# Optimization experiments

Hardware: AMD Instinct MI355X
Metric: run time of the kernel (lower is better)

## Reference

```python
import jax, jax.numpy as jnp
import numpy as np

N_NODES = 10000
DEG = 16
E = N_NODES * DEG
IN = 256
OUT = 256
B = 2
SLOPE = 0.2


def setup_inputs() -> dict:
    key = jax.random.key(0)
    ks = jax.random.split(key, 8)
    rng = np.random.default_rng(0)
    # edges sorted by source, every node appears as a source exactly DEG times
    src = np.repeat(np.arange(N_NODES, dtype=np.int64), DEG)
    tgt = rng.integers(0, N_NODES, size=E).astype(np.int64)
    # torch.unique(..., return_inverse=True) -> sorted uniques + inverse ids
    usrc, sid = np.unique(src, return_inverse=True)
    utgt, tid = np.unique(tgt, return_inverse=True)
    s = 1.0 / np.sqrt(IN)
    sa = 1.0 / np.sqrt(2 * OUT)
    return {
        "nodes": jax.random.normal(ks[0], (N_NODES, B, IN), jnp.float32),
        "Ws": jax.random.normal(ks[1], (IN, OUT), jnp.float32) * s,
        "bs": jnp.zeros((OUT,), jnp.float32),
        "Wt": jax.random.normal(ks[2], (IN, OUT), jnp.float32) * s,
        "bt": jnp.zeros((OUT,), jnp.float32),
        "Wv": jax.random.normal(ks[3], (IN, OUT), jnp.float32) * s,
        "bv": jnp.zeros((OUT,), jnp.float32),
        "Wa": jax.random.normal(ks[4], (2 * OUT, 1), jnp.float32) * sa,
        "ba": jnp.zeros((1,), jnp.float32),
        "unique_source_node_id": jnp.asarray(usrc),
        "unique_target_node_id": jnp.asarray(utgt),
        "source_id_per_edge": jnp.asarray(sid),
        "target_id_per_edge": jnp.asarray(tid),
    }


def reference(nodes, Ws, bs, Wt, bt, Wv, bv, Wa, ba,
              unique_source_node_id, unique_target_node_id,
              source_id_per_edge, target_id_per_edge):
    Ns = unique_source_node_id.shape[0]
    # project_node_states
    src_proj = nodes[unique_source_node_id] @ Ws + bs          # [Ns, B, O]
    tgt_proj = nodes[unique_target_node_id] @ Wt + bt          # [Nt, B, O]
    # gather_node_pairs + attention + LeakyReLU
    paired = jnp.concatenate(
        [src_proj[source_id_per_edge], tgt_proj[target_id_per_edge]], axis=-1)  # [E, B, 2O]
    scores = jax.nn.leaky_relu(paired @ Wa + ba, SLOPE)        # [E, B, 1]
    # neighbourhood_softmax: exp(clip) then scatter-add over source segments
    ex = jnp.exp(jnp.clip(scores, -2.0, 2.0))
    denom = jax.ops.segment_sum(ex, source_id_per_edge, num_segments=Ns)
    alpha = ex / denom[source_id_per_edge]                     # [E, B, 1]
    # apply_attention (values_type='new')
    vals = nodes[unique_target_node_id] @ Wv + bv              # [Nt, B, O]
    weighted = alpha * vals[target_id_per_edge]                # [E, B, O]
    # aggregate_neighbours: the original indexes the per-edge weighted values
    # by target_id_per_edge along the EDGE axis (faithfully reproduced), then
    # sums contiguous same-source segments.
    gathered = weighted[target_id_per_edge]                    # [E, B, O]
    agg = jax.ops.segment_sum(gathered, source_id_per_edge, num_segments=Ns)
    # update_sources (update_type='sum'), return_only_source_nodes=True
    return src_proj + agg                                      # [Ns, B, O]
```

## Files before the change

### kernel.cpp

```cpp
#include <hip/hip_runtime.h>

#define B2 2
#define DEG 16
#define SLOPE 0.2f

typedef __attribute__((ext_vector_type(8))) short short8;
typedef __attribute__((ext_vector_type(8))) unsigned short ushort8;
typedef __attribute__((ext_vector_type(4))) unsigned short ushort4v;
typedef __attribute__((ext_vector_type(4))) float f32x4;

__device__ inline unsigned short f2bf(float f) {
  union { float f; unsigned u; } v; v.f = f;
  unsigned r = v.u + 0x7fff + ((v.u >> 16) & 1);
  return (unsigned short)(r >> 16);
}
__device__ inline float bf2f(unsigned short u) {
  union { unsigned u; float f; } c; c.u = ((unsigned)u) << 16;
  return c.f;
}

__device__ inline float wave_dot256(const float* __restrict__ a,
                                    const float* __restrict__ b, int lane) {
  float4 x = *(const float4*)(a + lane * 4);
  float4 y = *(const float4*)(b + lane * 4);
  float v = x.x * y.x + x.y * y.y + x.z * y.z + x.w * y.w;
  #pragma unroll
  for (int off = 32; off; off >>= 1) v += __shfl_down(v, off);
  return v;
}

__global__ __launch_bounds__(256) void prep_w_k(
    const float* __restrict__ Ws, const float* __restrict__ Wt,
    const float* __restrict__ Wv, const float* __restrict__ Wa,
    const float* __restrict__ bs, const float* __restrict__ bt,
    unsigned short* __restrict__ WsT, unsigned short* __restrict__ WvT,
    float* __restrict__ ws_comb, float* __restrict__ wt_comb,
    float* __restrict__ consts) {
  int bx = blockIdx.x;
  if (bx < 32) {
    const float* src = (bx & 16) ? Wv : Ws;
    unsigned short* dst = (bx & 16) ? WvT : WsT;
    int rc = bx & 15;
    int r0 = (rc >> 2) * 64, c0 = (rc & 3) * 64;
    __shared__ float tile[64][65];
    int tr = threadIdx.x >> 6, tc = threadIdx.x & 63;
    #pragma unroll
    for (int i = 0; i < 16; ++i) {
      int r = tr * 16 + i;
      tile[r][tc] = src[(long)(r0 + r) * 256 + c0 + tc];
    }
    __syncthreads();
    #pragma unroll
    for (int i = 0; i < 16; ++i) {
      int r = tr * 16 + i;
      dst[(long)(c0 + r) * 256 + r0 + tc] = f2bf(tile[tc][r]);
    }
  } else {
    int wave = (bx - 32) * 4 + (threadIdx.x >> 6);
    int lane = threadIdx.x & 63;
    if (wave >= 514) return;
    const float *vec, *wa;
    float* dst;
    if (wave < 256)       { vec = Ws + (long)wave * 256;         wa = Wa;       dst = ws_comb + wave; }
    else if (wave < 512)  { vec = Wt + (long)(wave - 256) * 256; wa = Wa + 256; dst = wt_comb + (wave - 256); }
    else if (wave == 512) { vec = bs; wa = Wa;       dst = consts; }
    else                  { vec = bt; wa = Wa + 256; dst = consts + 1; }
    float v = wave_dot256(vec, wa, lane);
    if (lane == 0) *dst = v;
  }
}

__global__ __launch_bounds__(256) void prep_nodes_k(
    const float* __restrict__ nodes, const float* __restrict__ ws_comb,
    const float* __restrict__ wt_comb, unsigned short* __restrict__ nodes_bf,
    float* __restrict__ an_s, float* __restrict__ an_t, int nrows) {
  int wave = blockIdx.x * 4 + (threadIdx.x >> 6);
  int lane = threadIdx.x & 63;
  if (wave >= nrows) return;
  const float4 a = *(const float4*)(nodes + (long)wave * 256 + lane * 4);
  ushort4v p;
  p[0] = f2bf(a.x); p[1] = f2bf(a.y); p[2] = f2bf(a.z); p[3] = f2bf(a.w);
  *(ushort4v*)(nodes_bf + (long)wave * 256 + lane * 4) = p;
  const float4 w1 = *(const float4*)(ws_comb + lane * 4);
  const float4 w2 = *(const float4*)(wt_comb + lane * 4);
  float vs = a.x * w1.x + a.y * w1.y + a.z * w1.z + a.w * w1.w;
  float vt = a.x * w2.x + a.y * w2.y + a.z * w2.z + a.w * w2.w;
  #pragma unroll
  for (int off = 32; off; off >>= 1) {
    vs += __shfl_down(vs, off);
    vt += __shfl_down(vt, off);
  }
  if (lane == 0) { an_s[wave] = vs; an_t[wave] = vt; }
}

__global__ __launch_bounds__(256, 2) void gemm_mfma_k(
    const unsigned short* __restrict__ Abf,
    const int* __restrict__ usrc, const int* __restrict__ utgt,
    const unsigned short* __restrict__ WsT, const unsigned short* __restrict__ WvT,
    const float* __restrict__ bs, const float* __restrict__ bv,
    unsigned short* __restrict__ sproj_bf, unsigned short* __restrict__ vals_bf,
    const float* __restrict__ an_s, const float* __restrict__ an_t,
    const int* __restrict__ tid_arr, const float* __restrict__ consts,
    const float* __restrict__ ba, float* __restrict__ alpha,
    int Ms, int Mt, int Ns) {
  if (blockIdx.z == 2) {
    if (blockIdx.y != 0) return;
    int g = blockIdx.x * 256 + threadIdx.x;
    int s = g >> 1, b = g & 1;
    if (s >= Ns) return;
    float base = an_s[(long)usrc[s] * B2 + b] + consts[0] + consts[1] + ba[0];
    float ex[DEG];
    float den = 0.f;
    #pragma unroll
    for (int j = 0; j < DEG; ++j) {
      int t = tid_arr[s * DEG + j];
      float sc = base + an_t[(long)utgt[t] * B2 + b];
      sc = sc > 0.f ? sc : SLOPE * sc;
      sc = fminf(2.f, fmaxf(-2.f, sc));
      float ev = __expf(sc);
      ex[j] = ev;
      den += ev;
    }
    float inv = 1.f / den;
    #pragma unroll
    for (int j = 0; j < DEG; ++j) alpha[(long)(s * DEG + j) * B2 + b] = ex[j] * inv;
    return;
  }
  bool second = blockIdx.z != 0;
  const int* idx = second ? utgt : usrc;
  const unsigned short* WT = second ? WvT : WsT;
  const float* bias = second ? bv : bs;
  unsigned short* dstC = second ? vals_bf : sproj_bf;
  int M = second ? Mt : Ms;
  int row0 = blockIdx.x * 128, col0 = blockIdx.y * 128;
  if (row0 >= M) return;

  constexpr int LDT = 72;
  __shared__ unsigned short As[128 * LDT];
  __shared__ unsigned short Bs[128 * LDT];
  int t = threadIdx.x;
  int wv = t >> 6, lane = t & 63;
  int srow = t >> 3;
  int scol = (t & 7) * 8;
  const unsigned short* ap[4];
  #pragma unroll
  for (int p = 0; p < 4; ++p) {
    int m = row0 + srow + 32 * p;
    int mc = m < M ? m : M - 1;
    long ar = (long)idx[mc >> 1] * B2 + (mc & 1);
    ap[p] = Abf + ar * 256 + scol;
  }
  const unsigned short* bp[4];
  #pragma unroll
  for (int q = 0; q < 4; ++q)
    bp[q] = WT + (long)(col0 + srow + 32 * q) * 256 + scol;

  f32x4 acc[2][8];
  #pragma unroll
  for (int i = 0; i < 2; ++i)
    #pragma unroll
    for (int j = 0; j < 8; ++j) acc[i][j] = (f32x4)(0.f);

  for (int k0 = 0; k0 < 256; k0 += 64) {
    ushort8 av[4], bvv[4];
    #pragma unroll
    for (int p = 0; p < 4; ++p) av[p] = *(const ushort8*)(ap[p] + k0);
    #pragma unroll
    for (int q = 0; q < 4; ++q) bvv[q] = *(const ushort8*)(bp[q] + k0);
    __syncthreads();
    #pragma unroll
    for (int p = 0; p < 4; ++p)
      *(ushort8*)&As[(srow + 32 * p) * LDT + scol] = av[p];
    #pragma unroll
    for (int q = 0; q < 4; ++q)
      *(ushort8*)&Bs[(srow + 32 * q) * LDT + scol] = bvv[q];
    __syncthreads();
    #pragma unroll
    for (int ks = 0; ks < 64; ks += 32) {
      int ko = ks + (lane >> 4) * 8;
      short8 af0 = *(const short8*)&As[(32 * wv + (lane & 15)) * LDT + ko];
      short8 af1 = *(const short8*)&As[(32 * wv + 16 + (lane & 15)) * LDT + ko];
      #pragma unroll
      for (int j = 0; j < 8; ++j) {
        short8 bf = *(const short8*)&Bs[(16 * j + (lane & 15)) * LDT + ko];
        acc[0][j] = __builtin_amdgcn_mfma_f32_16x16x32_bf16(af0, bf, acc[0][j], 0, 0, 0);
        acc[1][j] = __builtin_amdgcn_mfma_f32_16x16x32_bf16(af1, bf, acc[1][j], 0, 0, 0);
      }
    }
  }
  int cq = lane >> 4;
  #pragma unroll
  for (int j = 0; j < 8; ++j) {
    int col = col0 + 16 * j + (lane & 15);
    float bval = bias[col];
    #pragma unroll
    for (int i = 0; i < 2; ++i) {
      #pragma unroll
      for (int r = 0; r < 4; ++r) {
        int row = row0 + 32 * wv + 16 * i + cq * 4 + r;
        if (row < M)
          dstC[(long)row * 256 + col] = f2bf(acc[i][j][r] + bval);
      }
    }
  }
}

__global__ __launch_bounds__(256) void aggregate_k(
    const unsigned short* __restrict__ sproj, const unsigned short* __restrict__ vals,
    const float* __restrict__ alpha, const int* __restrict__ tid_arr,
    float* __restrict__ out, int Ns) {
  int s = blockIdx.x * 4 + (threadIdx.x >> 6);
  int lane = threadIdx.x & 63;
  if (s >= Ns) return;
  int f = tid_arr[s * DEG + (lane & 15)];
  int b = lane >> 5;
  float al = alpha[(long)f * B2 + b];
  int t2 = tid_arr[f];
  ushort8 sp = *(const ushort8*)(sproj + (long)s * 512 + lane * 8);
  float acc[8];
  #pragma unroll
  for (int k = 0; k < 8; ++k) acc[k] = bf2f(sp[k]);
  #pragma unroll
  for (int j = 0; j < DEG; ++j) {
    int rr = __shfl(t2, j);
    float aj = __shfl(al, (lane & 32) + j);
    ushort8 v = *(const ushort8*)(vals + (long)rr * 512 + lane * 8);
    #pragma unroll
    for (int k = 0; k < 8; ++k) acc[k] += aj * bf2f(v[k]);
  }
  long ob = (long)s * 512 + lane * 8;
  float4 p0, p1;
  p0.x = acc[0]; p0.y = acc[1]; p0.z = acc[2]; p0.w = acc[3];
  p1.x = acc[4]; p1.y = acc[5]; p1.z = acc[6]; p1.w = acc[7];
  *(float4*)(out + ob) = p0;
  *(float4*)(out + ob + 4) = p1;
}

extern "C" void kernel_launch(void* const* d_in, const int* in_sizes, int n_in,
                              void* d_out, int out_size, void* d_ws, size_t ws_size,
                              hipStream_t stream) {
  const float* nodes = (const float*)d_in[0];
  const float* Ws = (const float*)d_in[1];
  const float* bs = (const float*)d_in[2];
  const float* Wt = (const float*)d_in[3];
  const float* bt = (const float*)d_in[4];
  const float* Wv = (const float*)d_in[5];
  const float* bv = (const float*)d_in[6];
  const float* Wa = (const float*)d_in[7];
  const float* ba = (const float*)d_in[8];
  const int* usrc = (const int*)d_in[9];
  const int* utgt = (const int*)d_in[10];
  const int* tidp = (const int*)d_in[12];
  int Ns = in_sizes[9], Nt = in_sizes[10];
  int NsB = Ns * B2, NtB = Nt * B2;
  long nrows = in_sizes[0] / 256;

  unsigned short* nodes_bf = (unsigned short*)d_ws;
  unsigned short* WsT = nodes_bf + nrows * 256;
  unsigned short* WvT = WsT + 65536;
  unsigned short* vals_bf = WvT + 65536;
  unsigned short* sproj_bf = vals_bf + (size_t)NtB * 256;
  float* fbase = (float*)(sproj_bf + (size_t)NsB * 256);
  float* an_s = fbase;
  float* an_t = an_s + nrows;
  float* ws_comb = an_t + nrows;
  float* wt_comb = ws_comb + 256;
  float* consts = wt_comb + 256;
  float* alpha = consts + 16;
  float* out = (float*)d_out;

  prep_w_k<<<161, 256, 0, stream>>>(Ws, Wt, Wv, Wa, bs, bt,
                                    WsT, WvT, ws_comb, wt_comb, consts);
  prep_nodes_k<<<(int)((nrows + 3) / 4), 256, 0, stream>>>(
      nodes, ws_comb, wt_comb, nodes_bf, an_s, an_t, (int)nrows);
  int maxM = NsB > NtB ? NsB : NtB;
  gemm_mfma_k<<<dim3((maxM + 127) / 128, 2, 3), 256, 0, stream>>>(
      nodes_bf, usrc, utgt, WsT, WvT, bs, bv, sproj_bf, vals_bf,
      an_s, an_t, tidp, consts, ba, alpha, NsB, NtB, Ns);
  aggregate_k<<<(Ns + 3) / 4, 256, 0, stream>>>(
      sproj_bf, vals_bf, alpha, tidp, out, Ns);
}
```

Baseline: 135.3 us.

## Prefetch next K tile in GEMM, vectorize epilogue stores, nontemporal aggregate IO

```diff
diff --git a/kernel.cpp b/kernel.cpp
--- a/kernel.cpp
+++ b/kernel.cpp
@@ -161,12 +161,14 @@
     #pragma unroll
     for (int j = 0; j < 8; ++j) acc[i][j] = (f32x4)(0.f);
 
+  ushort8 av[4], bvv[4];
+  #pragma unroll
+  for (int p = 0; p < 4; ++p) av[p] = *(const ushort8*)(ap[p]);
+  #pragma unroll
+  for (int q = 0; q < 4; ++q) bvv[q] = *(const ushort8*)(bp[q]);
+
+  #pragma unroll
   for (int k0 = 0; k0 < 256; k0 += 64) {
-    ushort8 av[4], bvv[4];
-    #pragma unroll
-    for (int p = 0; p < 4; ++p) av[p] = *(const ushort8*)(ap[p] + k0);
-    #pragma unroll
-    for (int q = 0; q < 4; ++q) bvv[q] = *(const ushort8*)(bp[q] + k0);
     __syncthreads();
     #pragma unroll
     for (int p = 0; p < 4; ++p)
@@ -175,6 +177,12 @@
     for (int q = 0; q < 4; ++q)
       *(ushort8*)&Bs[(srow + 32 * q) * LDT + scol] = bvv[q];
     __syncthreads();
+    if (k0 < 192) {
+      #pragma unroll
+      for (int p = 0; p < 4; ++p) av[p] = *(const ushort8*)(ap[p] + k0 + 64);
+      #pragma unroll
+      for (int q = 0; q < 4; ++q) bvv[q] = *(const ushort8*)(bp[q] + k0 + 64);
+    }
     #pragma unroll
     for (int ks = 0; ks < 64; ks += 32) {
       int ko = ks + (lane >> 4) * 8;
@@ -183,23 +191,26 @@
       #pragma unroll
       for (int j = 0; j < 8; ++j) {
         short8 bf = *(const short8*)&Bs[(16 * j + (lane & 15)) * LDT + ko];
-        acc[0][j] = __builtin_amdgcn_mfma_f32_16x16x32_bf16(af0, bf, acc[0][j], 0, 0, 0);
-        acc[1][j] = __builtin_amdgcn_mfma_f32_16x16x32_bf16(af1, bf, acc[1][j], 0, 0, 0);
+        acc[0][j] = __builtin_amdgcn_mfma_f32_16x16x32_bf16(bf, af0, acc[0][j], 0, 0, 0);
+        acc[1][j] = __builtin_amdgcn_mfma_f32_16x16x32_bf16(bf, af1, acc[1][j], 0, 0, 0);
       }
     }
   }
-  int cq = lane >> 4;
+  int cq = lane >> 4, rl = lane & 15;
   #pragma unroll
   for (int j = 0; j < 8; ++j) {
-    int col = col0 + 16 * j + (lane & 15);
-    float bval = bias[col];
+    int col = col0 + 16 * j + 4 * cq;
+    float4 b4 = *(const float4*)(bias + col);
     #pragma unroll
     for (int i = 0; i < 2; ++i) {
-      #pragma unroll
-      for (int r = 0; r < 4; ++r) {
-        int row = row0 + 32 * wv + 16 * i + cq * 4 + r;
-        if (row < M)
-          dstC[(long)row * 256 + col] = f2bf(acc[i][j][r] + bval);
+      int row = row0 + 32 * wv + 16 * i + rl;
+      if (row < M) {
+        ushort4v p;
+        p[0] = f2bf(acc[i][j][0] + b4.x);
+        p[1] = f2bf(acc[i][j][1] + b4.y);
+        p[2] = f2bf(acc[i][j][2] + b4.z);
+        p[3] = f2bf(acc[i][j][3] + b4.w);
+        *(ushort4v*)(dstC + (long)row * 256 + col) = p;
       }
     }
   }
@@ -216,7 +227,8 @@
   int b = lane >> 5;
   float al = alpha[(long)f * B2 + b];
   int t2 = tid_arr[f];
-  ushort8 sp = *(const ushort8*)(sproj + (long)s * 512 + lane * 8);
+  ushort8 sp = __builtin_nontemporal_load(
+      (const ushort8*)(sproj + (long)s * 512 + lane * 8));
   float acc[8];
   #pragma unroll
   for (int k = 0; k < 8; ++k) acc[k] = bf2f(sp[k]);
@@ -229,11 +241,11 @@
     for (int k = 0; k < 8; ++k) acc[k] += aj * bf2f(v[k]);
   }
   long ob = (long)s * 512 + lane * 8;
-  float4 p0, p1;
-  p0.x = acc[0]; p0.y = acc[1]; p0.z = acc[2]; p0.w = acc[3];
-  p1.x = acc[4]; p1.y = acc[5]; p1.z = acc[6]; p1.w = acc[7];
-  *(float4*)(out + ob) = p0;
-  *(float4*)(out + ob + 4) = p1;
+  f32x4 p0, p1;
+  p0[0] = acc[0]; p0[1] = acc[1]; p0[2] = acc[2]; p0[3] = acc[3];
+  p1[0] = acc[4]; p1[1] = acc[5]; p1[2] = acc[6]; p1[3] = acc[7];
+  __builtin_nontemporal_store(p0, (f32x4*)(out + ob));
+  __builtin_nontemporal_store(p1, (f32x4*)(out + ob + 4));
 }
 
 extern "C" void kernel_launch(void* const* d_in, const int* in_sizes, int n_in,
```

New measurement: 128.9 us. -4.8%, faster.
